# Optimization experiments

Measured on AMD Instinct MI355X. Metric: run time of the kernel, lower is better.

The kernel has to match this reference:

```python
import jax, jax.numpy as jnp
import numpy as np

B, T, DIM, H, HD = 2, 2048, 1024, 8, 128
ATTN_SCALE = 0.12  # attn_args.attn_scale (modded-nanogpt constant)
F32_EPS = float(np.finfo(np.float32).eps)  # F.rms_norm default eps


def ste_round(x):
    # straight-through round (round_grad_pt): identity gradient
    return x + jax.lax.stop_gradient(jnp.round(x) - x)


def quantized_linear(x, num_bits=8, eps=1e-5):
    num_steps = (2 ** num_bits - 1) // 2  # 127
    xnmin = jnp.minimum(jnp.min(x, -1, keepdims=True), -eps)
    xpmax = jnp.maximum(jnp.max(x, -1, keepdims=True), eps)
    xp = ste_round(x / xpmax * num_steps) / num_steps * xpmax
    xn = ste_round(x / xnmin * num_steps) / num_steps * xnmin
    return jnp.where(x >= 0, xp, xn)


def ternary_quantize_mean_special(w):
    # w: [3, hdim, dim]; per-leading-slice scale
    s = jnp.maximum(jnp.mean(jnp.mean(jnp.abs(w), -1, keepdims=True), -2, keepdims=True), 1e-5)
    return s * jnp.clip(ste_round(w / s), -1.0, 1.0)


def ternary_quantize(w):
    s = jnp.maximum(jnp.mean(jnp.abs(w)), 1e-5)
    return s * jnp.clip(ste_round(w / s), -1.0, 1.0)


def rmsnorm(x):
    return x * jax.lax.rsqrt(jnp.mean(x * x, -1, keepdims=True) + F32_EPS)


def rotary(x, cos, sin):
    # x: [B,T,H,HD]; cos,sin: [T, HD//2]
    x1, x2 = jnp.split(x, 2, axis=-1)
    c = cos[None, :, None, :]
    s = sin[None, :, None, :]
    return jnp.concatenate([x1 * c + x2 * s, -x1 * s + x2 * c], axis=-1)


def setup_inputs() -> dict:
    key = jax.random.key(0)
    ks = jax.random.split(key, 5)
    x = jax.random.normal(ks[0], (B, T, DIM), jnp.float32)
    ve = jax.random.normal(ks[1], (B, T, DIM), jnp.float32)
    sa_lambdas = jnp.array([0.5, 0.5], jnp.float32)
    inv_freq = 1.0 / (10000.0 ** (np.arange(0, HD, 2, dtype=np.float32) / HD))
    ang = np.arange(T, dtype=np.float32)[:, None] * inv_freq[None, :]
    cos = jnp.asarray(np.cos(ang), jnp.float32)
    sin = jnp.asarray(np.sin(ang), jnp.float32)
    bound = (3.0 ** 0.5) * 0.5 * DIM ** (-0.5)
    qkvo_w = jax.random.uniform(ks[2], (4, H * HD, DIM), jnp.float32, -bound, bound)
    gate_w = 0.1 * jax.random.normal(ks[3], (H, 12), jnp.float32)
    return {"x": x, "ve": ve, "sa_lambdas": sa_lambdas, "cos": cos, "sin": sin,
            "qkvo_w": qkvo_w, "gate_w": gate_w}


def reference(x, ve, sa_lambdas, cos, sin, qkvo_w, gate_w):
    # pre-activation int8 fake-quant (ENABLE_ATTN_PRE_ACT_QUANTIZATION)
    xq = quantized_linear(x, num_bits=8)
    # ternary-quantized QKV weights (ENABLE_ATTN_QUANTIZATION)
    w_qkv = ternary_quantize_mean_special(qkvo_w[:3]).reshape(3 * H * HD, DIM)
    qkv = jnp.einsum('btd,ed->bte', xq, w_qkv).reshape(B, T, 3 * H, HD)
    q, k, v = qkv[:, :, :H], qkv[:, :, H:2 * H], qkv[:, :, 2 * H:]
    q, k = rmsnorm(q), rmsnorm(k)
    q, k = rotary(q, cos, sin), rotary(k, cos, sin)
    v = sa_lambdas[0] * v + sa_lambdas[1] * ve.reshape(v.shape)
    # q/k int8 fake-quant (ENABLE_ATTN_ACT_QUANTIZATION)
    q = quantized_linear(q, num_bits=8)
    k = quantized_linear(k, num_bits=8)
    # causal SDPA with explicit scale
    scores = jnp.einsum('bqhd,bkhd->bhqk', q, k) * ATTN_SCALE
    mask = jnp.tril(jnp.ones((T, T), bool))
    scores = jnp.where(mask[None, None], scores, -jnp.inf)
    p = jax.nn.softmax(scores, axis=-1)
    y = jnp.einsum('bhqk,bkhd->bqhd', p, v)  # [B,T,H,HD]
    # sigmoid gate from first 12 features of (quantized) x
    gate = jax.nn.sigmoid(jnp.einsum('btf,hf->bth', xq[..., :12], gate_w))
    y = (y * gate[..., None]).reshape(B, T, H * HD)
    # ternary-quantized output projection (ENABLE_ATTN_PROJ_QUANTIZATION)
    w_o = ternary_quantize(qkvo_w[3])
    return jnp.einsum('bte,de->btd', y, w_o)
```

## Files before the change

### kernel.cpp

```cpp
#include <hip/hip_runtime.h>
#include <hip/hip_bf16.h>
#include <cstddef>
#include <cstdint>

#define B_    2
#define T_    2048
#define DIM_  1024
#define H_    8
#define HD_   128
#define BT_   (B_*T_)
#define E3_   (3*H_*HD_)
#define F32_EPS_ 1.1920929e-07f
#define QSC_  0.17312340490667562f

typedef __attribute__((ext_vector_type(8))) short bh8_t;
typedef __attribute__((ext_vector_type(4))) float f32x4_t;
typedef __attribute__((ext_vector_type(16))) float f32x16_t;
typedef __attribute__((ext_vector_type(4))) unsigned short us4_t;

__device__ inline unsigned short bf16r(float f) {
    unsigned u = __builtin_bit_cast(unsigned, f);
    u = (u + 0x7fffu + ((u >> 16) & 1u)) >> 16;
    return (unsigned short)u;
}
__device__ inline float b2f(unsigned short u) {
    return __builtin_bit_cast(float, (unsigned)u << 16);
}
__device__ inline unsigned cvtpk(float a, float b) {
    unsigned r;
    asm("v_cvt_pk_bf16_f32 %0, %1, %2" : "=v"(r) : "v"(a), "v"(b));
    return r;
}
__device__ inline void gl16(const unsigned short* g, unsigned short* l) {
    __builtin_amdgcn_global_load_lds((const __attribute__((address_space(1))) void*)g,
                                     (__attribute__((address_space(3))) void*)l, 16, 0, 0);
}

__global__ __launch_bounds__(256) void absmean1_kernel(const float* __restrict__ w, float* __restrict__ partial) {
    int blk = blockIdx.x;
    size_t off = (size_t)blk * 4096;
    __shared__ float red[256];
    int tid = threadIdx.x;
    float acc = 0.f;
    const float* p = w + off + tid*16;
    #pragma unroll
    for (int j = 0; j < 4; j++) {
        float4 v = *(const float4*)(p + j*4);
        acc += fabsf(v.x) + fabsf(v.y) + fabsf(v.z) + fabsf(v.w);
    }
    red[tid] = acc; __syncthreads();
    for (int s = 128; s > 0; s >>= 1) { if (tid < s) red[tid] += red[tid+s]; __syncthreads(); }
    if (tid == 0) partial[blk] = red[0];
}

__global__ __launch_bounds__(256) void absmean2_kernel(const float* __restrict__ partial, float* __restrict__ scales) {
    int m = blockIdx.x;
    __shared__ float red[256];
    int tid = threadIdx.x;
    red[tid] = partial[m*256 + tid]; __syncthreads();
    for (int s = 128; s > 0; s >>= 1) { if (tid < s) red[tid] += red[tid+s]; __syncthreads(); }
    if (tid == 0) scales[m] = fmaxf(red[0] / (float)(DIM_*DIM_), 1e-5f);
}

__global__ __launch_bounds__(256) void quant_w_kernel(const float* __restrict__ w, const float* __restrict__ scales,
                                                      unsigned short* __restrict__ wq) {
    int base = (blockIdx.x * 256 + threadIdx.x) * 8;
    float s = scales[base >> 20];
    float inv = 1.f / s;
    unsigned short out[8];
    float4 v0 = *(const float4*)(w + base);
    float4 v1 = *(const float4*)(w + base + 4);
    float t[8] = {v0.x, v0.y, v0.z, v0.w, v1.x, v1.y, v1.z, v1.w};
    #pragma unroll
    for (int j = 0; j < 8; j++) {
        float r = rintf(t[j] * inv);
        r = fminf(1.f, fmaxf(-1.f, r));
        out[j] = (r == 0.f) ? 0 : (r > 0.f ? 0x3F80 : 0xBF80);
    }
    *(int4*)(wq + base) = *(const int4*)out;
}

__global__ __launch_bounds__(256) void quant_x_gate_kernel(const float* __restrict__ x, const float* __restrict__ gw,
                                                           unsigned short* __restrict__ xqb, float* __restrict__ gate) {
    int row = blockIdx.x;
    const float* xr = x + (size_t)row * DIM_;
    unsigned short* qr = xqb + (size_t)row * DIM_;
    __shared__ float red[256];
    __shared__ float x12[12];
    int tid = threadIdx.x;
    float v[4];
    float mn = 1e30f, mx = -1e30f;
    #pragma unroll
    for (int i = 0; i < 4; i++) {
        v[i] = xr[i*256 + tid];
        mn = fminf(mn, v[i]); mx = fmaxf(mx, v[i]);
    }
    red[tid] = mn; __syncthreads();
    for (int s = 128; s > 0; s >>= 1) { if (tid < s) red[tid] = fminf(red[tid], red[tid+s]); __syncthreads(); }
    mn = red[0]; __syncthreads();
    red[tid] = mx; __syncthreads();
    for (int s = 128; s > 0; s >>= 1) { if (tid < s) red[tid] = fmaxf(red[tid], red[tid+s]); __syncthreads(); }
    mx = red[0]; __syncthreads();
    float p = fmaxf(mx, 1e-5f);
    float n = fminf(mn, -1e-5f);
    #pragma unroll
    for (int i = 0; i < 4; i++) {
        int gi = i*256 + tid;
        float xv = v[i];
        float sc = (xv >= 0.f) ? p : n;
        float q = rintf(xv / sc * 127.f) / 127.f * sc;
        qr[gi] = bf16r(q);
        if (gi < 12) x12[gi] = q;
    }
    __syncthreads();
    if (tid < H_) {
        float acc = 0.f;
        #pragma unroll
        for (int f = 0; f < 12; f++) acc += x12[f] * gw[tid*12 + f];
        gate[(size_t)row * H_ + tid] = 1.f / (1.f + expf(-acc));
    }
}

template<int MT, bool OBF>
__global__ __launch_bounds__(256) void gemm_bf16_kernel(const unsigned short* __restrict__ A,
                                                        const unsigned short* __restrict__ Bm,
                                                        const float* __restrict__ sw, int sbase,
                                                        void* __restrict__ Cv, int M, int N, int K) {
    __shared__ __align__(16) unsigned short As[MT*32*64];
    __shared__ __align__(16) unsigned short Bs[128*64];
    int bm = blockIdx.y * (MT*32), bn = blockIdx.x * 128;
    int tid = threadIdx.x;
    int w = tid >> 6, l = tid & 63;
    int wr = w >> 1, wc = w & 1;
    int lg = l >> 4, lq = l & 15;
    f32x4_t acc[MT][4];
    #pragma unroll
    for (int mt = 0; mt < MT; mt++)
        #pragma unroll
        for (int nt = 0; nt < 4; nt++) acc[mt][nt] = (f32x4_t)0.f;

    for (int k0 = 0; k0 < K; k0 += 64) {
        #pragma unroll
        for (int i = 0; i < MT; i++) {
            int ob = (i*4 + w) << 10;
            int o  = ob + (l << 4);
            int row = o >> 7;
            int lcn = ((o >> 4) & 7) ^ (row & 7);
            gl16(A + (size_t)(bm+row)*K + k0 + lcn*8, (unsigned short*)As + (ob >> 1));
        }
        #pragma unroll
        for (int i = 0; i < 4; i++) {
            int ob = (i*4 + w) << 10;
            int o  = ob + (l << 4);
            int row = o >> 7;
            int lcn = ((o >> 4) & 7) ^ (row & 7);
            gl16(Bm + (size_t)(bn+row)*K + k0 + lcn*8, (unsigned short*)Bs + (ob >> 1));
        }
        __syncthreads();
        #pragma unroll
        for (int kk = 0; kk < 2; kk++) {
            bh8_t af[MT], bf[4];
            #pragma unroll
            for (int mt = 0; mt < MT; mt++) {
                int r = wr*(MT*16) + mt*16 + lq;
                int j = kk*4 + lg;
                af[mt] = *(const bh8_t*)(As + r*64 + (((j ^ (r & 7)))<<3));
            }
            #pragma unroll
            for (int nt = 0; nt < 4; nt++) {
                int r = wc*64 + nt*16 + lq;
                int j = kk*4 + lg;
                bf[nt] = *(const bh8_t*)(Bs + r*64 + (((j ^ (r & 7)))<<3));
            }
            #pragma unroll
            for (int mt = 0; mt < MT; mt++)
                #pragma unroll
                for (int nt = 0; nt < 4; nt++)
                    acc[mt][nt] = __builtin_amdgcn_mfma_f32_16x16x32_bf16(af[mt], bf[nt], acc[mt][nt], 0, 0, 0);
        }
        __syncthreads();
    }
    #pragma unroll
    for (int nt = 0; nt < 4; nt++) {
        int col = bn + wc*64 + nt*16 + lq;
        float s = sw[sbase + (col >> 10)];
        #pragma unroll
        for (int mt = 0; mt < MT; mt++) {
            int row = bm + wr*(MT*16) + mt*16 + lg*4;
            #pragma unroll
            for (int r = 0; r < 4; r++) {
                if constexpr (OBF)
                    ((unsigned short*)Cv)[(size_t)(row + r)*N + col] = bf16r(acc[mt][nt][r] * s);
                else
                    ((float*)Cv)[(size_t)(row + r)*N + col] = acc[mt][nt][r] * s;
            }
        }
    }
}

__global__ __launch_bounds__(256) void qkv_post_kernel(const unsigned short* __restrict__ qkvb,
                                                       const float* __restrict__ ve,
                                                       const float* __restrict__ lam,
                                                       const float* __restrict__ cosb, const float* __restrict__ sinb,
                                                       unsigned short* __restrict__ Qb, unsigned short* __restrict__ Kb,
                                                       unsigned short* __restrict__ Vb) {
    int bt = blockIdx.x;
    int b = bt >> 11, t = bt & (T_ - 1);
    int w = threadIdx.x >> 6, l = threadIdx.x & 63;
    const unsigned short* base = qkvb + (size_t)bt * E3_;
    float l0 = lam[0], l1 = lam[1];
    #pragma unroll
    for (int i = 0; i < 2; i++) {
        int h = w*2 + i;
        const unsigned short* row = base + (16 + h)*HD_;
        const float* ver = ve + (size_t)bt*DIM_ + h*HD_;
        unsigned short* dst = Vb + ((size_t)(b*H_+h)*T_ + t)*HD_;
        dst[l]      = bf16r(l0*b2f(row[l])    + l1*ver[l]);
        dst[l + 64] = bf16r(l0*b2f(row[l+64]) + l1*ver[l+64]);
    }
    float cc = cosb[(size_t)t*64 + l], ss = sinb[(size_t)t*64 + l];
    #pragma unroll
    for (int i = 0; i < 4; i++) {
        int part = w*4 + i;
        const unsigned short* row = base + part*HD_;
        float x1 = b2f(row[l]), x2 = b2f(row[l+64]);
        float ssq = x1*x1 + x2*x2;
        #pragma unroll
        for (int off = 1; off < 64; off <<= 1) ssq += __shfl_xor(ssq, off);
        float rms = 1.0f / sqrtf(ssq / 128.0f + F32_EPS_);
        x1 *= rms; x2 *= rms;
        float o1 = x1*cc + x2*ss;
        float o2 = -x1*ss + x2*cc;
        float mn = fminf(o1, o2), mx = fmaxf(o1, o2);
        #pragma unroll
        for (int off = 1; off < 64; off <<= 1) {
            mn = fminf(mn, __shfl_xor(mn, off));
            mx = fmaxf(mx, __shfl_xor(mx, off));
        }
        float p = fmaxf(mx, 1e-5f);
        float n = fminf(mn, -1e-5f);
        float s1 = (o1 >= 0.f) ? p : n;
        float s2 = (o2 >= 0.f) ? p : n;
        float q1 = rintf(o1 / s1 * 127.f) / 127.f * s1;
        float q2 = rintf(o2 / s2 * 127.f) / 127.f * s2;
        if (part < 8) {
            unsigned short* dst = Qb + ((size_t)(b*H_+part)*T_ + t)*HD_;
            dst[l] = bf16r(QSC_ * q1); dst[l + 64] = bf16r(QSC_ * q2);
        } else {
            unsigned short* dst = Kb + ((size_t)(b*H_+part-8)*T_ + t)*HD_;
            dst[l] = bf16r(q1); dst[l + 64] = bf16r(q2);
        }
    }
}

__global__ __launch_bounds__(256) void transpose_v_kernel(const unsigned short* __restrict__ Vb,
                                                          unsigned short* __restrict__ VT) {
    int tt = blockIdx.x;
    int dt = blockIdx.y;
    int bh = blockIdx.z;
    __shared__ unsigned short L[64][80];
    int tid = threadIdx.x;
    #pragma unroll
    for (int i = 0; i < 2; i++) {
        int c = tid + i*256;
        int r = c >> 3, dc = c & 7;
        int4 v = *(const int4*)(Vb + ((size_t)bh*T_ + tt*64 + r)*HD_ + dt*64 + dc*8);
        *(int4*)(&L[r][dc*8]) = v;
    }
    __syncthreads();
    #pragma unroll
    for (int i = 0; i < 2; i++) {
        int c = tid + i*256;
        int r = c >> 3, tc = c & 7;
        unsigned short tmp[8];
        #pragma unroll
        for (int jj = 0; jj < 8; jj++) tmp[jj] = L[tc*8+jj][r];
        *(int4*)(VT + ((size_t)bh*HD_ + dt*64 + r)*T_ + tt*64 + tc*8) = *(const int4*)tmp;
    }
}

__global__ __launch_bounds__(256) void attn_kernel(const unsigned short* __restrict__ Qb,
                                                   const unsigned short* __restrict__ Kb,
                                                   const unsigned short* __restrict__ VT,
                                                   const float* __restrict__ gate,
                                                   unsigned short* __restrict__ Yb) {
    __shared__ __align__(16) unsigned char SMEM[65536];
    int id = blockIdx.x;
    int bh = id & 15;
    int qi = id >> 4;
    int qt = (qi < 16) ? (31 - qi) : (qi - 16);
    int b = bh >> 3, h = bh & 7;
    int tid = threadIdx.x;
    int w = tid >> 6, l = tid & 63;
    int qsub = w >> 1, qq = w & 1;
    int hh = l >> 5, l5 = l & 31;
    int qrow = qsub*32 + l5;
    int qg = qt*64 + qrow;

    const unsigned short* Kbase = Kb + (size_t)bh*T_*HD_;
    const unsigned short* Vbase = VT + (size_t)bh*HD_*T_;
    const unsigned short* Qg = Qb + ((size_t)bh*T_ + (size_t)qt*64) * HD_;

    bh8_t qf[8];
    #pragma unroll
    for (int ks = 0; ks < 8; ks++)
        qf[ks] = *(const bh8_t*)(Qg + (size_t)qrow*HD_ + ks*16 + hh*8);

    int nr = qt + 1;

    f32x16_t o0 = (f32x16_t)0.f, o1 = (f32x16_t)0.f, o2 = (f32x16_t)0.f, o3 = (f32x16_t)0.f;
    float mrun = -1e20f, lrun = 0.f;

#define STAGE(BI, J) { \
    unsigned short* kb_ = (unsigned short*)(SMEM + (BI)*16384); \
    unsigned short* vb_ = (unsigned short*)(SMEM + 32768 + (BI)*16384); \
    _Pragma("unroll") \
    for (int i_ = 0; i_ < 4; i_++) { \
        int ob_ = (i_*4 + w) << 10; \
        int o_  = ob_ + (l << 4); \
        int rk_ = o_ >> 8; \
        int lk_ = ((o_ >> 4) & 15) ^ (rk_ & 15); \
        gl16(Kbase + (size_t)((J)*64 + rk_)*HD_ + lk_*8, kb_ + (ob_ >> 1)); \
        int rv_ = o_ >> 7; \
        int lv_ = ((o_ >> 4) & 7) ^ (rv_ & 7); \
        gl16(Vbase + (size_t)rv_*T_ + (J)*64 + lv_*8, vb_ + (ob_ >> 1)); \
    } }

    STAGE(0, 0);
    for (int j = 0; j < nr; j++) {
        if (j + 1 < nr) {
            STAGE((j+1) & 1, j+1);
            asm volatile("s_waitcnt vmcnt(8)" ::: "memory");
        } else {
            asm volatile("s_waitcnt vmcnt(0)" ::: "memory");
        }
        __builtin_amdgcn_s_barrier();
        asm volatile("" ::: "memory");
        const unsigned short* kb = (const unsigned short*)(SMEM + (j&1)*16384);
        const unsigned short* vb = (const unsigned short*)(SMEM + 32768 + (j&1)*16384);
        int kvb = j*64 + qq*32;
        if (kvb <= qt*64 + qsub*32 + 31) {
            f32x16_t s = (f32x16_t)0.f;
            int krow = qq*32 + l5;
            __builtin_amdgcn_s_setprio(1);
            #pragma unroll
            for (int ks = 0; ks < 8; ks++) {
                int c = (ks*2 + hh) ^ (krow & 15);
                bh8_t kf = *(const bh8_t*)(kb + krow*128 + c*8);
                s = __builtin_amdgcn_mfma_f32_32x32x16_bf16(kf, qf[ks], s, 0, 0, 0);
            }
            __builtin_amdgcn_s_setprio(0);
            if (kvb + 31 > qt*64 + qsub*32) {
                #pragma unroll
                for (int r = 0; r < 16; r++) {
                    int key = kvb + (r & 3) + 8*(r >> 2) + 4*hh;
                    if (key > qg) s[r] = -1e30f;
                }
            }
            float t8[8], t4[4];
            #pragma unroll
            for (int r = 0; r < 8; r++) t8[r] = fmaxf(s[2*r], s[2*r+1]);
            #pragma unroll
            for (int r = 0; r < 4; r++) t4[r] = fmaxf(t8[2*r], t8[2*r+1]);
            float tm = fmaxf(fmaxf(t4[0], t4[1]), fmaxf(t4[2], t4[3]));
            tm = fmaxf(tm, __shfl_xor(tm, 32));
            if (!__all(tm - mrun <= 8.f)) {
                float mnew = fmaxf(mrun, tm);
                float scf = __builtin_amdgcn_exp2f(mrun - mnew);
                lrun *= scf;
                o0 *= scf; o1 *= scf; o2 *= scf; o3 *= scf;
                mrun = mnew;
            }
            float p[16];
            #pragma unroll
            for (int r = 0; r < 16; r++) p[r] = __builtin_amdgcn_exp2f(s[r] - mrun);
            #pragma unroll
            for (int r = 0; r < 8; r++) t8[r] = p[2*r] + p[2*r+1];
            #pragma unroll
            for (int r = 0; r < 4; r++) t4[r] = t8[2*r] + t8[2*r+1];
            float ls = (t4[0] + t4[1]) + (t4[2] + t4[3]);
            ls += __shfl_xor(ls, 32);
            lrun += ls;
            unsigned u0 = cvtpk(p[0], p[1]),   u1 = cvtpk(p[2], p[3]);
            unsigned u2 = cvtpk(p[4], p[5]),   u3 = cvtpk(p[6], p[7]);
            unsigned u4 = cvtpk(p[8], p[9]),   u5 = cvtpk(p[10], p[11]);
            unsigned u6 = cvtpk(p[12], p[13]), u7 = cvtpk(p[14], p[15]);
            unsigned x0 = (unsigned)__shfl_xor((int)u0, 32), x1 = (unsigned)__shfl_xor((int)u1, 32);
            unsigned x2 = (unsigned)__shfl_xor((int)u2, 32), x3 = (unsigned)__shfl_xor((int)u3, 32);
            unsigned x4 = (unsigned)__shfl_xor((int)u4, 32), x5 = (unsigned)__shfl_xor((int)u5, 32);
            unsigned x6 = (unsigned)__shfl_xor((int)u6, 32), x7 = (unsigned)__shfl_xor((int)u7, 32);
            union { bh8_t v; unsigned uu[4]; } B0, B1;
            B0.uu[0] = hh ? x2 : u0;  B0.uu[1] = hh ? x3 : u1;
            B0.uu[2] = hh ? u2 : x0;  B0.uu[3] = hh ? u3 : x1;
            B1.uu[0] = hh ? x6 : u4;  B1.uu[1] = hh ? x7 : u5;
            B1.uu[2] = hh ? u6 : x4;  B1.uu[3] = hh ? u7 : x5;
            __builtin_amdgcn_s_setprio(1);
#define PV_STEP(DT, OACC) { \
    int vrow = DT*32 + l5; \
    bh8_t vf0 = *(const bh8_t*)(vb + vrow*64 + (((qq*4 + hh) ^ (vrow & 7))<<3)); \
    OACC = __builtin_amdgcn_mfma_f32_32x32x16_bf16(vf0, B0.v, OACC, 0, 0, 0); \
    bh8_t vf1 = *(const bh8_t*)(vb + vrow*64 + (((qq*4 + 2 + hh) ^ (vrow & 7))<<3)); \
    OACC = __builtin_amdgcn_mfma_f32_32x32x16_bf16(vf1, B1.v, OACC, 0, 0, 0); }
            PV_STEP(0, o0) PV_STEP(1, o1) PV_STEP(2, o2) PV_STEP(3, o3)
#undef PV_STEP
            __builtin_amdgcn_s_setprio(0);
        }
        asm volatile("s_waitcnt lgkmcnt(0)" ::: "memory");
        __builtin_amdgcn_s_barrier();
        asm volatile("" ::: "memory");
    }

    f32x16_t oA[4] = {o0, o1, o2, o3};
    float* OB = (float*)SMEM;
    float* ML = (float*)(SMEM + 32768);
    unsigned short* YS = (unsigned short*)(SMEM + 33280);
    if (qq != 0) {
        float* obuf = OB + (size_t)qsub * 4096;
        #pragma unroll
        for (int dt = 0; dt < 4; dt++)
            #pragma unroll
            for (int g = 0; g < 4; g++) {
                f32x4_t v4;
                #pragma unroll
                for (int e = 0; e < 4; e++) v4[e] = oA[dt][g*4+e];
                int ch = (dt*4 + g) ^ (l & 7);
                *(f32x4_t*)(obuf + l*64 + ch*4) = v4;
            }
        if (hh == 0) {
            ML[(qsub*32 + l5)*2]     = mrun;
            ML[(qsub*32 + l5)*2 + 1] = lrun;
        }
    }
    __syncthreads();
    if (qq == 0) {
        float mb = ML[(qsub*32 + l5)*2];
        float lb = ML[(qsub*32 + l5)*2 + 1];
        float mN = fmaxf(mrun, mb);
        float fa = __builtin_amdgcn_exp2f(mrun - mN), fb = __builtin_amdgcn_exp2f(mb - mN);
        const float* obuf = OB + (size_t)qsub * 4096;
        #pragma unroll
        for (int dt = 0; dt < 4; dt++)
            #pragma unroll
            for (int g = 0; g < 4; g++) {
                int ch = (dt*4 + g) ^ (l & 7);
                f32x4_t v4 = *(const f32x4_t*)(obuf + l*64 + ch*4);
                #pragma unroll
                for (int e = 0; e < 4; e++)
                    oA[dt][g*4+e] = oA[dt][g*4+e]*fa + v4[e]*fb;
            }
        lrun = lrun*fa + lb*fb;
        float gv = gate[((size_t)b*T_ + (size_t)qg)*H_ + h];
        float inv = gv / lrun;
        #pragma unroll
        for (int dt = 0; dt < 4; dt++)
            #pragma unroll
            for (int g = 0; g < 4; g++) {
                unsigned short pk4[4];
                #pragma unroll
                for (int e = 0; e < 4; e++) pk4[e] = bf16r(oA[dt][g*4+e] * inv);
                int ch = (dt*4 + g) ^ (qrow & 7);
                *(us4_t*)(YS + (size_t)qrow*128 + ch*8 + hh*4) = *(const us4_t*)pk4;
            }
    }
    __syncthreads();
    #pragma unroll
    for (int i = 0; i < 4; i++) {
        int idx = tid + i*256;
        int r = idx >> 4, scn = idx & 15;
        int lcn = scn ^ (r & 7);
        int4 v = *(const int4*)(YS + (size_t)r*128 + scn*8);
        *(int4*)(Yb + (size_t)(b*T_ + qt*64 + r)*DIM_ + h*HD_ + lcn*8) = v;
    }
#undef STAGE
}

extern "C" void kernel_launch(void* const* d_in, const int* in_sizes, int n_in,
                              void* d_out, int out_size, void* d_ws, size_t ws_size,
                              hipStream_t stream) {
    const float* x    = (const float*)d_in[0];
    const float* ve   = (const float*)d_in[1];
    const float* lam  = (const float*)d_in[2];
    const float* cosb = (const float*)d_in[3];
    const float* sinb = (const float*)d_in[4];
    const float* qkvo = (const float*)d_in[5];
    const float* gw   = (const float*)d_in[6];

    char* ws = (char*)d_ws;
    float* scales  = (float*)ws;
    float* partial = scales + 16;
    unsigned short* WQb  = (unsigned short*)(ws + (1<<13));
    unsigned short* XQb  = WQb + (size_t)4*DIM_*DIM_;
    unsigned short* QKVb = XQb + (size_t)BT_*DIM_;
    float* GT = (float*)(QKVb + (size_t)BT_*E3_);
    unsigned short* Qb = (unsigned short*)(GT + (size_t)BT_*H_);
    unsigned short* Kb = Qb + (size_t)B_*H_*T_*HD_;
    unsigned short* VT = Kb + (size_t)B_*H_*T_*HD_;
    unsigned short* Vb = VT + (size_t)B_*H_*T_*HD_;
    unsigned short* Yb = QKVb;

    absmean1_kernel<<<1024, 256, 0, stream>>>(qkvo, partial);
    absmean2_kernel<<<4, 256, 0, stream>>>(partial, scales);
    quant_w_kernel<<<(4*DIM_*DIM_)/(256*8), 256, 0, stream>>>(qkvo, scales, WQb);
    quant_x_gate_kernel<<<BT_, 256, 0, stream>>>(x, gw, XQb, GT);
    gemm_bf16_kernel<4, true><<<dim3(E3_/128, BT_/128), 256, 0, stream>>>(XQb, WQb, scales, 0, QKVb, BT_, E3_, DIM_);
    qkv_post_kernel<<<BT_, 256, 0, stream>>>(QKVb, ve, lam, cosb, sinb, Qb, Kb, Vb);
    transpose_v_kernel<<<dim3(T_/64, HD_/64, B_*H_), 256, 0, stream>>>(Vb, VT);
    attn_kernel<<<512, 256, 0, stream>>>(Qb, Kb, VT, GT, Yb);
    gemm_bf16_kernel<2, false><<<dim3(DIM_/128, BT_/64), 256, 0, stream>>>(Yb, WQb + (size_t)3*DIM_*DIM_, scales, 3,
                                                                           (float*)d_out, BT_, DIM_, DIM_);
}
```

Measured before the change: 145.8 us.

## Split causal attention KV range into chunks with separate merge kernel

Splits each query tile's causal key range into chunks of up to 8 KV tiles, launching 1280 blocks instead of 512 so long-row tiles no longer dominate the tail. Multi-chunk tiles write bf16 partial outputs plus running max and sum to workspace, and a new merge kernel combines them with log-sum-exp weights and applies the gate. This aims to balance load across CUs and shorten the critical path. The cost is an extra launch, extra global traffic, and bf16 rounding of the partials before merging.

```diff
diff --git a/kernel.cpp b/kernel.cpp
--- a/kernel.cpp
+++ b/kernel.cpp
@@ -283,12 +283,19 @@
                                                    const unsigned short* __restrict__ Kb,
                                                    const unsigned short* __restrict__ VT,
                                                    const float* __restrict__ gate,
-                                                   unsigned short* __restrict__ Yb) {
+                                                   unsigned short* __restrict__ Yb,
+                                                   unsigned short* __restrict__ Opart,
+                                                   float* __restrict__ MLg) {
     __shared__ __align__(16) unsigned char SMEM[65536];
-    int id = blockIdx.x;
-    int bh = id & 15;
-    int qi = id >> 4;
-    int qt = (qi < 16) ? (31 - qi) : (qi - 16);
+    int rid = 1279 - (int)blockIdx.x;
+    int bh = rid & 15;
+    int idx = rid >> 4;
+    int qt, c, nc;
+    if (idx < 8)       { qt = idx;                 c = 0;           nc = 1; }
+    else if (idx < 24) { int t = idx - 8;  qt = 8  + (t >> 1);  c = t & 1;      nc = 2; }
+    else if (idx < 48) { int t = idx - 24; qt = 16 + t / 3;     c = t - 3*(t/3); nc = 3; }
+    else               { int t = idx - 48; qt = 24 + (t >> 2);  c = t & 3;      nc = 4; }
+    int pslot = (idx - 8)*16 + bh;
     int b = bh >> 3, h = bh & 7;
     int tid = threadIdx.x;
     int w = tid >> 6, l = tid & 63;
@@ -306,7 +313,9 @@
     for (int ks = 0; ks < 8; ks++)
         qf[ks] = *(const bh8_t*)(Qg + (size_t)qrow*HD_ + ks*16 + hh*8);
 
-    int nr = qt + 1;
+    int j0c  = c*8;
+    int jend = (qt + 1 < j0c + 8) ? (qt + 1) : (j0c + 8);
+    int ncr  = jend - j0c;
 
     f32x16_t o0 = (f32x16_t)0.f, o1 = (f32x16_t)0.f, o2 = (f32x16_t)0.f, o3 = (f32x16_t)0.f;
     float mrun = -1e20f, lrun = 0.f;
@@ -326,18 +335,19 @@
         gl16(Vbase + (size_t)rv_*T_ + (J)*64 + lv_*8, vb_ + (ob_ >> 1)); \
     } }
 
-    STAGE(0, 0);
-    for (int j = 0; j < nr; j++) {
-        if (j + 1 < nr) {
-            STAGE((j+1) & 1, j+1);
+    STAGE(0, j0c);
+    for (int jj = 0; jj < ncr; jj++) {
+        int j = j0c + jj;
+        if (jj + 1 < ncr) {
+            STAGE((jj+1) & 1, j+1);
             asm volatile("s_waitcnt vmcnt(8)" ::: "memory");
         } else {
             asm volatile("s_waitcnt vmcnt(0)" ::: "memory");
         }
         __builtin_amdgcn_s_barrier();
         asm volatile("" ::: "memory");
-        const unsigned short* kb = (const unsigned short*)(SMEM + (j&1)*16384);
-        const unsigned short* vb = (const unsigned short*)(SMEM + 32768 + (j&1)*16384);
+        const unsigned short* kb = (const unsigned short*)(SMEM + (jj&1)*16384);
+        const unsigned short* vb = (const unsigned short*)(SMEM + 32768 + (jj&1)*16384);
         int kvb = j*64 + qq*32;
         if (kvb <= qt*64 + qsub*32 + 31) {
             f32x16_t s = (f32x16_t)0.f;
@@ -345,8 +355,8 @@
             __builtin_amdgcn_s_setprio(1);
             #pragma unroll
             for (int ks = 0; ks < 8; ks++) {
-                int c = (ks*2 + hh) ^ (krow & 15);
-                bh8_t kf = *(const bh8_t*)(kb + krow*128 + c*8);
+                int cch = (ks*2 + hh) ^ (krow & 15);
+                bh8_t kf = *(const bh8_t*)(kb + krow*128 + cch*8);
                 s = __builtin_amdgcn_mfma_f32_32x32x16_bf16(kf, qf[ks], s, 0, 0, 0);
             }
             __builtin_amdgcn_s_setprio(0);
@@ -449,8 +459,18 @@
                     oA[dt][g*4+e] = oA[dt][g*4+e]*fa + v4[e]*fb;
             }
         lrun = lrun*fa + lb*fb;
-        float gv = gate[((size_t)b*T_ + (size_t)qg)*H_ + h];
-        float inv = gv / lrun;
+        mrun = mN;
+        float inv;
+        if (nc == 1) {
+            float gv = gate[((size_t)b*T_ + (size_t)qg)*H_ + h];
+            inv = gv / lrun;
+        } else {
+            inv = 1.f / lrun;
+            if (hh == 0) {
+                MLg[(size_t)pslot*128 + qrow*2]     = mrun;
+                MLg[(size_t)pslot*128 + qrow*2 + 1] = lrun;
+            }
+        }
         #pragma unroll
         for (int dt = 0; dt < 4; dt++)
             #pragma unroll
@@ -463,15 +483,85 @@
             }
     }
     __syncthreads();
-    #pragma unroll
-    for (int i = 0; i < 4; i++) {
-        int idx = tid + i*256;
-        int r = idx >> 4, scn = idx & 15;
-        int lcn = scn ^ (r & 7);
-        int4 v = *(const int4*)(YS + (size_t)r*128 + scn*8);
-        *(int4*)(Yb + (size_t)(b*T_ + qt*64 + r)*DIM_ + h*HD_ + lcn*8) = v;
+    if (nc == 1) {
+        #pragma unroll
+        for (int i = 0; i < 4; i++) {
+            int idx2 = tid + i*256;
+            int r = idx2 >> 4, scn = idx2 & 15;
+            int lcn = scn ^ (r & 7);
+            int4 v = *(const int4*)(YS + (size_t)r*128 + scn*8);
+            *(int4*)(Yb + (size_t)(b*T_ + qt*64 + r)*DIM_ + h*HD_ + lcn*8) = v;
+        }
+    } else {
+        unsigned short* od = Opart + (size_t)pslot*8192;
+        #pragma unroll
+        for (int i = 0; i < 4; i++) {
+            int idx2 = tid + i*256;
+            int r = idx2 >> 4, scn = idx2 & 15;
+            int lcn = scn ^ (r & 7);
+            int4 v = *(const int4*)(YS + (size_t)r*128 + scn*8);
+            *(int4*)(od + (size_t)r*128 + lcn*8) = v;
+        }
     }
 #undef STAGE
+}
+
+__global__ __launch_bounds__(256) void attn_merge_kernel(const unsigned short* __restrict__ Opart,
+                                                         const float* __restrict__ MLg,
+                                                         const float* __restrict__ gate,
+                                                         unsigned short* __restrict__ Yb) {
+    int mblk = blockIdx.x;
+    int bh = mblk & 15, ti = mblk >> 4;
+    int qt = 8 + ti;
+    int nc, base;
+    if (qt < 16)      { nc = 2; base = 8  + (qt - 8)*2;  }
+    else if (qt < 24) { nc = 3; base = 24 + (qt - 16)*3; }
+    else              { nc = 4; base = 48 + (qt - 24)*4; }
+    int b = bh >> 3, h = bh & 7;
+    int row = threadIdx.x >> 2;
+    int d0  = (threadIdx.x & 3) * 32;
+
+    float mc[4], lc[4];
+    float m = -1e30f;
+    #pragma unroll
+    for (int cc = 0; cc < 4; cc++) {
+        if (cc < nc) {
+            int ps = (base + cc - 8)*16 + bh;
+            mc[cc] = MLg[(size_t)ps*128 + row*2];
+            lc[cc] = MLg[(size_t)ps*128 + row*2 + 1];
+            m = fmaxf(m, mc[cc]);
+        }
+    }
+    float num[32];
+    #pragma unroll
+    for (int e = 0; e < 32; e++) num[e] = 0.f;
+    float den = 0.f;
+    #pragma unroll
+    for (int cc = 0; cc < 4; cc++) {
+        if (cc < nc) {
+            int ps = (base + cc - 8)*16 + bh;
+            float wgt = lc[cc] * __builtin_amdgcn_exp2f(mc[cc] - m);
+            den += wgt;
+            const unsigned short* op = Opart + (size_t)ps*8192 + row*128 + d0;
+            #pragma unroll
+            for (int e8 = 0; e8 < 4; e8++) {
+                union { int4 v; unsigned short q[8]; } u;
+                u.v = *(const int4*)(op + e8*8);
+                #pragma unroll
+                for (int k = 0; k < 8; k++) num[e8*8 + k] += wgt * b2f(u.q[k]);
+            }
+        }
+    }
+    float gv = gate[((size_t)b*T_ + qt*64 + row)*H_ + h];
+    float s = gv / den;
+    unsigned short* yd = Yb + (size_t)(b*T_ + qt*64 + row)*DIM_ + h*HD_ + d0;
+    #pragma unroll
+    for (int e8 = 0; e8 < 4; e8++) {
+        unsigned short pk8[8];
+        #pragma unroll
+        for (int k = 0; k < 8; k++) pk8[k] = bf16r(num[e8*8 + k] * s);
+        *(int4*)(yd + e8*8) = *(const int4*)pk8;
+    }
 }
 
 extern "C" void kernel_launch(void* const* d_in, const int* in_sizes, int n_in,
@@ -496,7 +586,9 @@
     unsigned short* Kb = Qb + (size_t)B_*H_*T_*HD_;
     unsigned short* VT = Kb + (size_t)B_*H_*T_*HD_;
     unsigned short* Vb = VT + (size_t)B_*H_*T_*HD_;
-    unsigned short* Yb = QKVb;
+    unsigned short* Yb = XQb;
+    unsigned short* Opart = QKVb;
+    float* MLg = (float*)(Opart + (size_t)1152*8192);
 
     absmean1_kernel<<<1024, 256, 0, stream>>>(qkvo, partial);
     absmean2_kernel<<<4, 256, 0, stream>>>(partial, scales);
@@ -505,7 +597,8 @@
     gemm_bf16_kernel<4, true><<<dim3(E3_/128, BT_/128), 256, 0, stream>>>(XQb, WQb, scales, 0, QKVb, BT_, E3_, DIM_);
     qkv_post_kernel<<<BT_, 256, 0, stream>>>(QKVb, ve, lam, cosb, sinb, Qb, Kb, Vb);
     transpose_v_kernel<<<dim3(T_/64, HD_/64, B_*H_), 256, 0, stream>>>(Vb, VT);
-    attn_kernel<<<512, 256, 0, stream>>>(Qb, Kb, VT, GT, Yb);
+    attn_kernel<<<1280, 256, 0, stream>>>(Qb, Kb, VT, GT, Yb, Opart, MLg);
+    attn_merge_kernel<<<384, 256, 0, stream>>>(Opart, MLg, GT, Yb);
     gemm_bf16_kernel<2, false><<<dim3(DIM_/128, BT_/64), 256, 0, stream>>>(Yb, WQb + (size_t)3*DIM_*DIM_, scales, 3,
                                                                            (float*)d_out, BT_, DIM_, DIM_);
 }
```

New measurement: 151.1 us. 3.6% more time.

## Split causal attention into per-wave key chunks with separate merge kernel

Applied to the files above, without the earlier changes.

Replaces the block-level attention that shared K/V tiles in LDS with independent per-wave work items, each handling 32 query rows over up to 16 key tiles read directly from global memory. Long query rows are split across up to four chunks whose partial outputs (bf16) and max/sum statistics go to workspace, then a new merge kernel combines them with the gate. The aim is better load balance and more parallelism across the causal triangle, but it gives up LDS reuse of K/V across waves, adds a second launch, and rounds the partials to bf16 before merging.

```diff
diff --git a/kernel.cpp b/kernel.cpp
--- a/kernel.cpp
+++ b/kernel.cpp
@@ -279,199 +279,225 @@
     }
 }
 
-__global__ __launch_bounds__(256) void attn_kernel(const unsigned short* __restrict__ Qb,
-                                                   const unsigned short* __restrict__ Kb,
-                                                   const unsigned short* __restrict__ VT,
-                                                   const float* __restrict__ gate,
-                                                   unsigned short* __restrict__ Yb) {
-    __shared__ __align__(16) unsigned char SMEM[65536];
-    int id = blockIdx.x;
-    int bh = id & 15;
-    int qi = id >> 4;
-    int qt = (qi < 16) ? (31 - qi) : (qi - 16);
-    int b = bh >> 3, h = bh & 7;
+__global__ __launch_bounds__(256, 4) void attn_kernel(const unsigned short* __restrict__ Qb,
+                                                      const unsigned short* __restrict__ Kb,
+                                                      const unsigned short* __restrict__ VT,
+                                                      const float* __restrict__ gate,
+                                                      unsigned short* __restrict__ Yb,
+                                                      unsigned short* __restrict__ Opart,
+                                                      float* __restrict__ MLg) {
+    __shared__ __align__(16) unsigned short YSm[4*4096];
     int tid = threadIdx.x;
     int w = tid >> 6, l = tid & 63;
-    int qsub = w >> 1, qq = w & 1;
+    int wid = blockIdx.x*4 + w;
+    int bh = wid / 160;
+    int g  = wid - bh*160;
+    int q32, c;
+    if (g < 16)      { q32 = g;                          c = 0; }
+    else if (g < 48) { int t = g-16; q32 = 16 + (t>>1);  c = t & 1; }
+    else if (g < 96) { int t = g-48; int q3 = t/3; q32 = 32 + q3; c = t - 3*q3; }
+    else             { int t = g-96; q32 = 48 + (t>>2);  c = t & 3; }
+    int nc = (q32 >> 4) + 1;
+    int s0 = c*16;
+    int send = min(s0 + 16, q32 + 1);
+    int b = bh >> 3, h = bh & 7;
     int hh = l >> 5, l5 = l & 31;
-    int qrow = qsub*32 + l5;
-    int qg = qt*64 + qrow;
+    int qg = q32*32 + l5;
 
     const unsigned short* Kbase = Kb + (size_t)bh*T_*HD_;
     const unsigned short* Vbase = VT + (size_t)bh*HD_*T_;
-    const unsigned short* Qg = Qb + ((size_t)bh*T_ + (size_t)qt*64) * HD_;
+    const unsigned short* Qg = Qb + ((size_t)bh*T_ + (size_t)q32*32) * HD_;
 
     bh8_t qf[8];
     #pragma unroll
     for (int ks = 0; ks < 8; ks++)
-        qf[ks] = *(const bh8_t*)(Qg + (size_t)qrow*HD_ + ks*16 + hh*8);
-
-    int nr = qt + 1;
+        qf[ks] = *(const bh8_t*)(Qg + (size_t)l5*HD_ + ks*16 + hh*8);
 
     f32x16_t o0 = (f32x16_t)0.f, o1 = (f32x16_t)0.f, o2 = (f32x16_t)0.f, o3 = (f32x16_t)0.f;
     float mrun = -1e20f, lrun = 0.f;
 
-#define STAGE(BI, J) { \
-    unsigned short* kb_ = (unsigned short*)(SMEM + (BI)*16384); \
-    unsigned short* vb_ = (unsigned short*)(SMEM + 32768 + (BI)*16384); \
-    _Pragma("unroll") \
-    for (int i_ = 0; i_ < 4; i_++) { \
-        int ob_ = (i_*4 + w) << 10; \
-        int o_  = ob_ + (l << 4); \
-        int rk_ = o_ >> 8; \
-        int lk_ = ((o_ >> 4) & 15) ^ (rk_ & 15); \
-        gl16(Kbase + (size_t)((J)*64 + rk_)*HD_ + lk_*8, kb_ + (ob_ >> 1)); \
-        int rv_ = o_ >> 7; \
-        int lv_ = ((o_ >> 4) & 7) ^ (rv_ & 7); \
-        gl16(Vbase + (size_t)rv_*T_ + (J)*64 + lv_*8, vb_ + (ob_ >> 1)); \
-    } }
-
-    STAGE(0, 0);
-    for (int j = 0; j < nr; j++) {
-        if (j + 1 < nr) {
-            STAGE((j+1) & 1, j+1);
-            asm volatile("s_waitcnt vmcnt(8)" ::: "memory");
-        } else {
-            asm volatile("s_waitcnt vmcnt(0)" ::: "memory");
-        }
-        __builtin_amdgcn_s_barrier();
-        asm volatile("" ::: "memory");
-        const unsigned short* kb = (const unsigned short*)(SMEM + (j&1)*16384);
-        const unsigned short* vb = (const unsigned short*)(SMEM + 32768 + (j&1)*16384);
-        int kvb = j*64 + qq*32;
-        if (kvb <= qt*64 + qsub*32 + 31) {
-            f32x16_t s = (f32x16_t)0.f;
-            int krow = qq*32 + l5;
-            __builtin_amdgcn_s_setprio(1);
-            #pragma unroll
-            for (int ks = 0; ks < 8; ks++) {
-                int c = (ks*2 + hh) ^ (krow & 15);
-                bh8_t kf = *(const bh8_t*)(kb + krow*128 + c*8);
-                s = __builtin_amdgcn_mfma_f32_32x32x16_bf16(kf, qf[ks], s, 0, 0, 0);
+    for (int s = s0; s < send; s++) {
+        int key0 = s*32;
+        bh8_t kf[8];
+        #pragma unroll
+        for (int ks = 0; ks < 8; ks++)
+            kf[ks] = *(const bh8_t*)(Kbase + (size_t)(key0 + l5)*HD_ + ks*16 + hh*8);
+        f32x16_t sA = (f32x16_t)0.f;
+        __builtin_amdgcn_s_setprio(1);
+        #pragma unroll
+        for (int ks = 0; ks < 8; ks++)
+            sA = __builtin_amdgcn_mfma_f32_32x32x16_bf16(kf[ks], qf[ks], sA, 0, 0, 0);
+        __builtin_amdgcn_s_setprio(0);
+        if (key0 + 31 > q32*32) {
+            #pragma unroll
+            for (int r = 0; r < 16; r++) {
+                int key = key0 + (r & 3) + 8*(r >> 2) + 4*hh;
+                if (key > qg) sA[r] = -1e30f;
             }
-            __builtin_amdgcn_s_setprio(0);
-            if (kvb + 31 > qt*64 + qsub*32) {
+        }
+        float t8[8], t4[4];
+        #pragma unroll
+        for (int r = 0; r < 8; r++) t8[r] = fmaxf(sA[2*r], sA[2*r+1]);
+        #pragma unroll
+        for (int r = 0; r < 4; r++) t4[r] = fmaxf(t8[2*r], t8[2*r+1]);
+        float tm = fmaxf(fmaxf(t4[0], t4[1]), fmaxf(t4[2], t4[3]));
+        tm = fmaxf(tm, __shfl_xor(tm, 32));
+        if (!__all(tm - mrun <= 8.f)) {
+            float mnew = fmaxf(mrun, tm);
+            float scf = __builtin_amdgcn_exp2f(mrun - mnew);
+            lrun *= scf;
+            o0 *= scf; o1 *= scf; o2 *= scf; o3 *= scf;
+            mrun = mnew;
+        }
+        float pp[16];
+        #pragma unroll
+        for (int r = 0; r < 16; r++) pp[r] = __builtin_amdgcn_exp2f(sA[r] - mrun);
+        #pragma unroll
+        for (int r = 0; r < 8; r++) t8[r] = pp[2*r] + pp[2*r+1];
+        #pragma unroll
+        for (int r = 0; r < 4; r++) t4[r] = t8[2*r] + t8[2*r+1];
+        float ls = (t4[0] + t4[1]) + (t4[2] + t4[3]);
+        ls += __shfl_xor(ls, 32);
+        lrun += ls;
+        unsigned u0 = cvtpk(pp[0], pp[1]),   u1 = cvtpk(pp[2], pp[3]);
+        unsigned u2 = cvtpk(pp[4], pp[5]),   u3 = cvtpk(pp[6], pp[7]);
+        unsigned u4 = cvtpk(pp[8], pp[9]),   u5 = cvtpk(pp[10], pp[11]);
+        unsigned u6 = cvtpk(pp[12], pp[13]), u7 = cvtpk(pp[14], pp[15]);
+        unsigned x0 = (unsigned)__shfl_xor((int)u0, 32), x1 = (unsigned)__shfl_xor((int)u1, 32);
+        unsigned x2 = (unsigned)__shfl_xor((int)u2, 32), x3 = (unsigned)__shfl_xor((int)u3, 32);
+        unsigned x4 = (unsigned)__shfl_xor((int)u4, 32), x5 = (unsigned)__shfl_xor((int)u5, 32);
+        unsigned x6 = (unsigned)__shfl_xor((int)u6, 32), x7 = (unsigned)__shfl_xor((int)u7, 32);
+        union { bh8_t v; unsigned uu[4]; } B0, B1;
+        B0.uu[0] = hh ? x2 : u0;  B0.uu[1] = hh ? x3 : u1;
+        B0.uu[2] = hh ? u2 : x0;  B0.uu[3] = hh ? u3 : x1;
+        B1.uu[0] = hh ? x6 : u4;  B1.uu[1] = hh ? x7 : u5;
+        B1.uu[2] = hh ? u6 : x4;  B1.uu[3] = hh ? u7 : x5;
+        bh8_t vf[8];
+        #pragma unroll
+        for (int dt = 0; dt < 4; dt++) {
+            vf[dt*2]   = *(const bh8_t*)(Vbase + (size_t)(dt*32 + l5)*T_ + key0 + hh*8);
+            vf[dt*2+1] = *(const bh8_t*)(Vbase + (size_t)(dt*32 + l5)*T_ + key0 + 16 + hh*8);
+        }
+        __builtin_amdgcn_s_setprio(1);
+        o0 = __builtin_amdgcn_mfma_f32_32x32x16_bf16(vf[0], B0.v, o0, 0, 0, 0);
+        o0 = __builtin_amdgcn_mfma_f32_32x32x16_bf16(vf[1], B1.v, o0, 0, 0, 0);
+        o1 = __builtin_amdgcn_mfma_f32_32x32x16_bf16(vf[2], B0.v, o1, 0, 0, 0);
+        o1 = __builtin_amdgcn_mfma_f32_32x32x16_bf16(vf[3], B1.v, o1, 0, 0, 0);
+        o2 = __builtin_amdgcn_mfma_f32_32x32x16_bf16(vf[4], B0.v, o2, 0, 0, 0);
+        o2 = __builtin_amdgcn_mfma_f32_32x32x16_bf16(vf[5], B1.v, o2, 0, 0, 0);
+        o3 = __builtin_amdgcn_mfma_f32_32x32x16_bf16(vf[6], B0.v, o3, 0, 0, 0);
+        o3 = __builtin_amdgcn_mfma_f32_32x32x16_bf16(vf[7], B1.v, o3, 0, 0, 0);
+        __builtin_amdgcn_s_setprio(0);
+    }
+
+    f32x16_t oA[4] = {o0, o1, o2, o3};
+    unsigned short* ys = YSm + w*4096;
+    float inv;
+    int pslot = 0;
+    if (nc == 1) {
+        float gv = gate[((size_t)b*T_ + (size_t)qg)*H_ + h];
+        inv = gv / lrun;
+    } else {
+        int off_;
+        if (q32 < 32)      off_ = (q32-16)*2;
+        else if (q32 < 48) off_ = 32 + (q32-32)*3;
+        else               off_ = 80 + (q32-48)*4;
+        pslot = (off_ + c)*16 + bh;
+        inv = 1.f / lrun;
+        if (hh == 0) {
+            MLg[(size_t)pslot*64 + l5*2]     = mrun;
+            MLg[(size_t)pslot*64 + l5*2 + 1] = lrun;
+        }
+    }
+    #pragma unroll
+    for (int dt = 0; dt < 4; dt++)
+        #pragma unroll
+        for (int gg = 0; gg < 4; gg++) {
+            unsigned short pk4[4];
+            #pragma unroll
+            for (int e = 0; e < 4; e++) pk4[e] = bf16r(oA[dt][gg*4+e] * inv);
+            int ch = (dt*4 + gg) ^ (l5 & 7);
+            *(us4_t*)(ys + (size_t)l5*128 + ch*8 + hh*4) = *(const us4_t*)pk4;
+        }
+    if (nc == 1) {
+        #pragma unroll
+        for (int i = 0; i < 8; i++) {
+            int idx = l + i*64;
+            int r = idx >> 4, scn = idx & 15;
+            int lcn = scn ^ (r & 7);
+            int4 v = *(const int4*)(ys + (size_t)r*128 + scn*8);
+            *(int4*)(Yb + (size_t)(b*T_ + q32*32 + r)*DIM_ + h*HD_ + lcn*8) = v;
+        }
+    } else {
+        unsigned short* od = Opart + (size_t)pslot*4096;
+        #pragma unroll
+        for (int i = 0; i < 8; i++) {
+            int idx = l + i*64;
+            int r = idx >> 4, scn = idx & 15;
+            int lcn = scn ^ (r & 7);
+            int4 v = *(const int4*)(ys + (size_t)r*128 + scn*8);
+            *(int4*)(od + (size_t)r*128 + lcn*8) = v;
+        }
+    }
+}
+
+__global__ __launch_bounds__(256) void attn_merge_kernel(const unsigned short* __restrict__ Opart,
+                                                         const float* __restrict__ MLg,
+                                                         const float* __restrict__ gate,
+                                                         unsigned short* __restrict__ Yb) {
+    int mblk = blockIdx.x;
+    int bh = mblk & 15;
+    int q32 = 16 + (mblk >> 4);
+    int nc = (q32 >> 4) + 1;
+    int off_;
+    if (q32 < 32)      off_ = (q32-16)*2;
+    else if (q32 < 48) off_ = 32 + (q32-32)*3;
+    else               off_ = 80 + (q32-48)*4;
+    int b = bh >> 3, h = bh & 7;
+    int row = threadIdx.x >> 3;
+    int d0  = (threadIdx.x & 7) * 16;
+
+    float mc[4], lc[4];
+    float m = -1e30f;
+    #pragma unroll
+    for (int cc = 0; cc < 4; cc++) {
+        if (cc < nc) {
+            int ps = (off_ + cc)*16 + bh;
+            mc[cc] = MLg[(size_t)ps*64 + row*2];
+            lc[cc] = MLg[(size_t)ps*64 + row*2 + 1];
+            m = fmaxf(m, mc[cc]);
+        }
+    }
+    float num[16];
+    #pragma unroll
+    for (int e = 0; e < 16; e++) num[e] = 0.f;
+    float den = 0.f;
+    #pragma unroll
+    for (int cc = 0; cc < 4; cc++) {
+        if (cc < nc) {
+            int ps = (off_ + cc)*16 + bh;
+            float wgt = lc[cc] * __builtin_amdgcn_exp2f(mc[cc] - m);
+            den += wgt;
+            const unsigned short* op = Opart + (size_t)ps*4096 + row*128 + d0;
+            #pragma unroll
+            for (int e8 = 0; e8 < 2; e8++) {
+                union { int4 v; unsigned short q[8]; } u;
+                u.v = *(const int4*)(op + e8*8);
                 #pragma unroll
-                for (int r = 0; r < 16; r++) {
-                    int key = kvb + (r & 3) + 8*(r >> 2) + 4*hh;
-                    if (key > qg) s[r] = -1e30f;
-                }
+                for (int k = 0; k < 8; k++) num[e8*8 + k] += wgt * b2f(u.q[k]);
             }
-            float t8[8], t4[4];
-            #pragma unroll
-            for (int r = 0; r < 8; r++) t8[r] = fmaxf(s[2*r], s[2*r+1]);
-            #pragma unroll
-            for (int r = 0; r < 4; r++) t4[r] = fmaxf(t8[2*r], t8[2*r+1]);
-            float tm = fmaxf(fmaxf(t4[0], t4[1]), fmaxf(t4[2], t4[3]));
-            tm = fmaxf(tm, __shfl_xor(tm, 32));
-            if (!__all(tm - mrun <= 8.f)) {
-                float mnew = fmaxf(mrun, tm);
-                float scf = __builtin_amdgcn_exp2f(mrun - mnew);
-                lrun *= scf;
-                o0 *= scf; o1 *= scf; o2 *= scf; o3 *= scf;
-                mrun = mnew;
-            }
-            float p[16];
-            #pragma unroll
-            for (int r = 0; r < 16; r++) p[r] = __builtin_amdgcn_exp2f(s[r] - mrun);
-            #pragma unroll
-            for (int r = 0; r < 8; r++) t8[r] = p[2*r] + p[2*r+1];
-            #pragma unroll
-            for (int r = 0; r < 4; r++) t4[r] = t8[2*r] + t8[2*r+1];
-            float ls = (t4[0] + t4[1]) + (t4[2] + t4[3]);
-            ls += __shfl_xor(ls, 32);
-            lrun += ls;
-            unsigned u0 = cvtpk(p[0], p[1]),   u1 = cvtpk(p[2], p[3]);
-            unsigned u2 = cvtpk(p[4], p[5]),   u3 = cvtpk(p[6], p[7]);
-            unsigned u4 = cvtpk(p[8], p[9]),   u5 = cvtpk(p[10], p[11]);
-            unsigned u6 = cvtpk(p[12], p[13]), u7 = cvtpk(p[14], p[15]);
-            unsigned x0 = (unsigned)__shfl_xor((int)u0, 32), x1 = (unsigned)__shfl_xor((int)u1, 32);
-            unsigned x2 = (unsigned)__shfl_xor((int)u2, 32), x3 = (unsigned)__shfl_xor((int)u3, 32);
-            unsigned x4 = (unsigned)__shfl_xor((int)u4, 32), x5 = (unsigned)__shfl_xor((int)u5, 32);
-            unsigned x6 = (unsigned)__shfl_xor((int)u6, 32), x7 = (unsigned)__shfl_xor((int)u7, 32);
-            union { bh8_t v; unsigned uu[4]; } B0, B1;
-            B0.uu[0] = hh ? x2 : u0;  B0.uu[1] = hh ? x3 : u1;
-            B0.uu[2] = hh ? u2 : x0;  B0.uu[3] = hh ? u3 : x1;
-            B1.uu[0] = hh ? x6 : u4;  B1.uu[1] = hh ? x7 : u5;
-            B1.uu[2] = hh ? u6 : x4;  B1.uu[3] = hh ? u7 : x5;
-            __builtin_amdgcn_s_setprio(1);
-#define PV_STEP(DT, OACC) { \
-    int vrow = DT*32 + l5; \
-    bh8_t vf0 = *(const bh8_t*)(vb + vrow*64 + (((qq*4 + hh) ^ (vrow & 7))<<3)); \
-    OACC = __builtin_amdgcn_mfma_f32_32x32x16_bf16(vf0, B0.v, OACC, 0, 0, 0); \
-    bh8_t vf1 = *(const bh8_t*)(vb + vrow*64 + (((qq*4 + 2 + hh) ^ (vrow & 7))<<3)); \
-    OACC = __builtin_amdgcn_mfma_f32_32x32x16_bf16(vf1, B1.v, OACC, 0, 0, 0); }
-            PV_STEP(0, o0) PV_STEP(1, o1) PV_STEP(2, o2) PV_STEP(3, o3)
-#undef PV_STEP
-            __builtin_amdgcn_s_setprio(0);
-        }
-        asm volatile("s_waitcnt lgkmcnt(0)" ::: "memory");
-        __builtin_amdgcn_s_barrier();
-        asm volatile("" ::: "memory");
-    }
-
-    f32x16_t oA[4] = {o0, o1, o2, o3};
-    float* OB = (float*)SMEM;
-    float* ML = (float*)(SMEM + 32768);
-    unsigned short* YS = (unsigned short*)(SMEM + 33280);
-    if (qq != 0) {
-        float* obuf = OB + (size_t)qsub * 4096;
-        #pragma unroll
-        for (int dt = 0; dt < 4; dt++)
-            #pragma unroll
-            for (int g = 0; g < 4; g++) {
-                f32x4_t v4;
-                #pragma unroll
-                for (int e = 0; e < 4; e++) v4[e] = oA[dt][g*4+e];
-                int ch = (dt*4 + g) ^ (l & 7);
-                *(f32x4_t*)(obuf + l*64 + ch*4) = v4;
-            }
-        if (hh == 0) {
-            ML[(qsub*32 + l5)*2]     = mrun;
-            ML[(qsub*32 + l5)*2 + 1] = lrun;
-        }
-    }
-    __syncthreads();
-    if (qq == 0) {
-        float mb = ML[(qsub*32 + l5)*2];
-        float lb = ML[(qsub*32 + l5)*2 + 1];
-        float mN = fmaxf(mrun, mb);
-        float fa = __builtin_amdgcn_exp2f(mrun - mN), fb = __builtin_amdgcn_exp2f(mb - mN);
-        const float* obuf = OB + (size_t)qsub * 4096;
-        #pragma unroll
-        for (int dt = 0; dt < 4; dt++)
-            #pragma unroll
-            for (int g = 0; g < 4; g++) {
-                int ch = (dt*4 + g) ^ (l & 7);
-                f32x4_t v4 = *(const f32x4_t*)(obuf + l*64 + ch*4);
-                #pragma unroll
-                for (int e = 0; e < 4; e++)
-                    oA[dt][g*4+e] = oA[dt][g*4+e]*fa + v4[e]*fb;
-            }
-        lrun = lrun*fa + lb*fb;
-        float gv = gate[((size_t)b*T_ + (size_t)qg)*H_ + h];
-        float inv = gv / lrun;
-        #pragma unroll
-        for (int dt = 0; dt < 4; dt++)
-            #pragma unroll
-            for (int g = 0; g < 4; g++) {
-                unsigned short pk4[4];
-                #pragma unroll
-                for (int e = 0; e < 4; e++) pk4[e] = bf16r(oA[dt][g*4+e] * inv);
-                int ch = (dt*4 + g) ^ (qrow & 7);
-                *(us4_t*)(YS + (size_t)qrow*128 + ch*8 + hh*4) = *(const us4_t*)pk4;
-            }
-    }
-    __syncthreads();
-    #pragma unroll
-    for (int i = 0; i < 4; i++) {
-        int idx = tid + i*256;
-        int r = idx >> 4, scn = idx & 15;
-        int lcn = scn ^ (r & 7);
-        int4 v = *(const int4*)(YS + (size_t)r*128 + scn*8);
-        *(int4*)(Yb + (size_t)(b*T_ + qt*64 + r)*DIM_ + h*HD_ + lcn*8) = v;
-    }
-#undef STAGE
+        }
+    }
+    float gv = gate[((size_t)b*T_ + q32*32 + row)*H_ + h];
+    float s = gv / den;
+    unsigned short* yd = Yb + (size_t)(b*T_ + q32*32 + row)*DIM_ + h*HD_ + d0;
+    #pragma unroll
+    for (int e8 = 0; e8 < 2; e8++) {
+        unsigned short pk8[8];
+        #pragma unroll
+        for (int k = 0; k < 8; k++) pk8[k] = bf16r(num[e8*8 + k] * s);
+        *(int4*)(yd + e8*8) = *(const int4*)pk8;
+    }
 }
 
 extern "C" void kernel_launch(void* const* d_in, const int* in_sizes, int n_in,
@@ -496,6 +522,8 @@
     unsigned short* Kb = Qb + (size_t)B_*H_*T_*HD_;
     unsigned short* VT = Kb + (size_t)B_*H_*T_*HD_;
     unsigned short* Vb = VT + (size_t)B_*H_*T_*HD_;
+    unsigned short* Opart = Vb + (size_t)B_*H_*T_*HD_;
+    float* MLg = (float*)(Opart + (size_t)2304*4096);
     unsigned short* Yb = QKVb;
 
     absmean1_kernel<<<1024, 256, 0, stream>>>(qkvo, partial);
@@ -505,7 +533,8 @@
     gemm_bf16_kernel<4, true><<<dim3(E3_/128, BT_/128), 256, 0, stream>>>(XQb, WQb, scales, 0, QKVb, BT_, E3_, DIM_);
     qkv_post_kernel<<<BT_, 256, 0, stream>>>(QKVb, ve, lam, cosb, sinb, Qb, Kb, Vb);
     transpose_v_kernel<<<dim3(T_/64, HD_/64, B_*H_), 256, 0, stream>>>(Vb, VT);
-    attn_kernel<<<512, 256, 0, stream>>>(Qb, Kb, VT, GT, Yb);
+    attn_kernel<<<640, 256, 0, stream>>>(Qb, Kb, VT, GT, Yb, Opart, MLg);
+    attn_merge_kernel<<<768, 256, 0, stream>>>(Opart, MLg, GT, Yb);
     gemm_bf16_kernel<2, false><<<dim3(DIM_/128, BT_/64), 256, 0, stream>>>(Yb, WQb + (size_t)3*DIM_*DIM_, scales, 3,
                                                                            (float*)d_out, BT_, DIM_, DIM_);
 }
```

Result: slower. 230.0 us (+57.8%).
